# Optimization experiments

Hardware: AMD Instinct MI355X
Metric: run time of the kernel (lower is better)

Reference implementation:

```python
import jax, jax.numpy as jnp
import numpy as np

B, S, D, H = 2, 2048, 1024, 16
HD = D // H

def setup_inputs() -> dict:
    key = jax.random.key(0)
    ks = jax.random.split(key, 5)
    s = 1.0 / np.sqrt(D)
    return {
        "x": jax.random.normal(ks[0], (B, S, D), dtype=jnp.float32),
        "Wq": jax.random.normal(ks[1], (D, D), dtype=jnp.float32) * s,
        "Wk": jax.random.normal(ks[2], (D, D), dtype=jnp.float32) * s,
        "Wv": jax.random.normal(ks[3], (D, D), dtype=jnp.float32) * s,
        "Wo": jax.random.normal(ks[4], (D, D), dtype=jnp.float32) * s,
        "bo": jnp.zeros((D,), dtype=jnp.float32),
    }

def reference(x, Wq, Wk, Wv, Wo, bo):
    b, n, _ = x.shape
    # QKV projections (no bias), reshape to [B, H, S, HD]
    def proj(W):
        return (x @ W.T).reshape(b, n, H, HD).transpose(0, 2, 1, 3)
    q, k, v = proj(Wq), proj(Wk), proj(Wv)
    scores = jnp.einsum("bhqd,bhkd->bhqk", q, k)
    causal = jnp.triu(jnp.ones((n, n), dtype=bool), k=1)
    scores = jnp.where(causal, -jnp.inf, scores)
    attn = jax.nn.softmax(scores / np.sqrt(HD), axis=-1)  # dropout p=0.0 (eval)
    ctx = jnp.einsum("bhqk,bhkd->bhqd", attn, v)
    ctx = ctx.transpose(0, 2, 1, 3).reshape(b, n, D)
    return ctx @ Wo.T + bo
```

## Files before the change

kernel.cpp:

```cpp
#include <hip/hip_runtime.h>
#include <stdint.h>


typedef __bf16 bf16_t;
typedef __bf16 bf16x8 __attribute__((ext_vector_type(8)));
typedef float  f32x4  __attribute__((ext_vector_type(4)));
typedef uint32_t u32x4 __attribute__((ext_vector_type(4)));

#define MFMA16(A, B, C) __builtin_amdgcn_mfma_f32_16x16x32_bf16(A, B, C, 0, 0, 0)

__device__ __forceinline__ void async_ld16(const bf16_t* g, bf16_t* l) {
  __builtin_amdgcn_global_load_lds(
      (const __attribute__((address_space(1))) void*)g,
      (__attribute__((address_space(3))) void*)l, 16, 0, 0);
}

__global__ __launch_bounds__(256) void cvt_all(
    const float* __restrict__ sx, const float* __restrict__ s1,
    const float* __restrict__ s2, const float* __restrict__ s3,
    bf16_t* __restrict__ dx, bf16_t* __restrict__ d1,
    bf16_t* __restrict__ d2, bf16_t* __restrict__ d3) {
  const int y = blockIdx.y;
  if (y != 0 && blockIdx.x >= 1024) return;
  const int i4 = (blockIdx.x * 256 + threadIdx.x) * 4;
  const float* s = (y == 0) ? sx : (y == 1) ? s1 : (y == 2) ? s2 : s3;
  bf16_t*      d = (y == 0) ? dx : (y == 1) ? d1 : (y == 2) ? d2 : d3;
  const float4 v = *(const float4*)(s + i4);
  union { uint64_t u; bf16_t h[4]; } pk;
  pk.h[0] = (bf16_t)v.x; pk.h[1] = (bf16_t)v.y;
  pk.h[2] = (bf16_t)v.z; pk.h[3] = (bf16_t)v.w;
  *(uint64_t*)(d + i4) = pk.u;
}

__global__ __launch_bounds__(256) void cvt_wo(
    const float* __restrict__ s, bf16_t* __restrict__ d) {
  const int i4 = (blockIdx.x * 256 + threadIdx.x) * 4;
  const float4 v = *(const float4*)(s + i4);
  union { uint64_t u; bf16_t h[4]; } pk;
  pk.h[0] = (bf16_t)v.x; pk.h[1] = (bf16_t)v.y;
  pk.h[2] = (bf16_t)v.z; pk.h[3] = (bf16_t)v.w;
  *(uint64_t*)(d + i4) = pk.u;
}

__global__ __launch_bounds__(256, 3) void gemm_qkv_a(
    const bf16_t* __restrict__ X,  const bf16_t* __restrict__ Wq,
    const bf16_t* __restrict__ Wk, const bf16_t* __restrict__ Wv,
    bf16_t* __restrict__ Q, bf16_t* __restrict__ K, bf16_t* __restrict__ V) {
  const int z = blockIdx.z;
  const bf16_t* W = (z == 0) ? Wq : (z == 1) ? Wk : Wv;
  bf16_t*       D = (z == 0) ? Q  : (z == 1) ? K  : V;
  const int mode = (z == 2) ? 1 : 0;

  __shared__ __align__(16) bf16_t As[128 * 64];
  __shared__ __align__(16) bf16_t Bs[128 * 64];

  const int tid  = threadIdx.x;
  const int lane = tid & 63;
  const int w    = tid >> 6;
  const int quad = lane >> 4;
  const int l15  = lane & 15;
  const int bm   = blockIdx.y * 128;
  const int bn   = blockIdx.x * 128;
  const int wm   = (w >> 1) * 64;
  const int wn   = (w & 1) * 64;
  const int sr   = lane >> 3;
  const int sc   = lane & 7;

  f32x4 acc[4][4] = {};

  for (int k0 = 0; k0 < 1024; k0 += 64) {
#pragma unroll
    for (int j = 0; j < 4; ++j) {
      const int r0 = w * 32 + j * 8;
      const int r  = r0 + sr;
      const int c  = sc ^ (r & 7);
      async_ld16(X + (size_t)(bm + r) * 1024 + k0 + c * 8, &As[r0 * 64]);
      async_ld16(W + (size_t)(bn + r) * 1024 + k0 + c * 8, &Bs[r0 * 64]);
    }
    __syncthreads();
#pragma unroll
    for (int kk = 0; kk < 64; kk += 32) {
      const int ck = (kk >> 3) + quad;
      bf16x8 aF[4], bF[4];
#pragma unroll
      for (int mt = 0; mt < 4; ++mt) {
        const int r = wm + mt * 16 + l15;
        aF[mt] = *(const bf16x8*)&As[r * 64 + (ck ^ (r & 7)) * 8];
      }
#pragma unroll
      for (int nt = 0; nt < 4; ++nt) {
        const int r = wn + nt * 16 + l15;
        bF[nt] = *(const bf16x8*)&Bs[r * 64 + (ck ^ (r & 7)) * 8];
      }
#pragma unroll
      for (int mt = 0; mt < 4; ++mt)
#pragma unroll
        for (int nt = 0; nt < 4; ++nt)
          acc[mt][nt] = MFMA16(aF[mt], bF[nt], acc[mt][nt]);
    }
    __syncthreads();
  }

#pragma unroll
  for (int mt = 0; mt < 4; ++mt) {
#pragma unroll
    for (int nt = 0; nt < 4; ++nt) {
      const int n  = bn + wn + nt * 16 + l15;
      const int mb = bm + wm + mt * 16 + quad * 4;
      const int h = n >> 6, hd = n & 63;
      if (mode == 0) {
#pragma unroll
        for (int r = 0; r < 4; ++r) {
          const int m = mb + r;
          const int b = m >> 11, s = m & 2047;
          D[(size_t)b * 2097152 + (size_t)h * 131072 + (size_t)s * 64 + hd] =
              (bf16_t)acc[mt][nt][r];
        }
      } else {
        const int b = mb >> 11, s0 = mb & 2047;
        union { uint64_t u; bf16_t h4[4]; } pk;
#pragma unroll
        for (int r = 0; r < 4; ++r) pk.h4[r] = (bf16_t)acc[mt][nt][r];
        *(uint64_t*)(D + (size_t)b * 2097152 + (size_t)h * 131072 +
                     (size_t)hd * 2048 + s0) = pk.u;
      }
    }
  }
}

__global__ __launch_bounds__(256, 2) void gemm_out_a(
    const bf16_t* __restrict__ ctx, const bf16_t* __restrict__ Wob,
    float* __restrict__ out, const float* __restrict__ bo) {
  __shared__ __align__(16) bf16_t As[64 * 64];
  __shared__ __align__(16) bf16_t Bs[128 * 64];

  const int tid  = threadIdx.x;
  const int lane = tid & 63;
  const int w    = tid >> 6;
  const int quad = lane >> 4;
  const int l15  = lane & 15;
  const int bm   = blockIdx.y * 64;
  const int bn   = blockIdx.x * 128;
  const int wm   = (w >> 1) * 32;
  const int wn   = (w & 1) * 64;
  const int sr   = lane >> 3;
  const int sc   = lane & 7;

  f32x4 acc[2][4] = {};

  for (int k0 = 0; k0 < 1024; k0 += 64) {
#pragma unroll
    for (int j = 0; j < 2; ++j) {
      const int r0 = w * 16 + j * 8;
      const int r  = r0 + sr;
      const int c  = sc ^ (r & 7);
      async_ld16(ctx + (size_t)(bm + r) * 1024 + k0 + c * 8, &As[r0 * 64]);
    }
#pragma unroll
    for (int j = 0; j < 4; ++j) {
      const int r0 = w * 32 + j * 8;
      const int r  = r0 + sr;
      const int c  = sc ^ (r & 7);
      async_ld16(Wob + (size_t)(bn + r) * 1024 + k0 + c * 8, &Bs[r0 * 64]);
    }
    __syncthreads();
#pragma unroll
    for (int kk = 0; kk < 64; kk += 32) {
      const int ck = (kk >> 3) + quad;
      bf16x8 aF[2], bF[4];
#pragma unroll
      for (int mt = 0; mt < 2; ++mt) {
        const int r = wm + mt * 16 + l15;
        aF[mt] = *(const bf16x8*)&As[r * 64 + (ck ^ (r & 7)) * 8];
      }
#pragma unroll
      for (int nt = 0; nt < 4; ++nt) {
        const int r = wn + nt * 16 + l15;
        bF[nt] = *(const bf16x8*)&Bs[r * 64 + (ck ^ (r & 7)) * 8];
      }
#pragma unroll
      for (int mt = 0; mt < 2; ++mt)
#pragma unroll
        for (int nt = 0; nt < 4; ++nt)
          acc[mt][nt] = MFMA16(aF[mt], bF[nt], acc[mt][nt]);
    }
    __syncthreads();
  }

#pragma unroll
  for (int mt = 0; mt < 2; ++mt) {
#pragma unroll
    for (int nt = 0; nt < 4; ++nt) {
      const int n  = bn + wn + nt * 16 + l15;
      const int mb = bm + wm + mt * 16 + quad * 4;
      const float bv = bo[n];
#pragma unroll
      for (int r = 0; r < 4; ++r)
        out[(size_t)(mb + r) * 1024 + n] = acc[mt][nt][r] + bv;
    }
  }
}

__global__ __launch_bounds__(256, 4) void attn(
    const bf16_t* __restrict__ Qw, const bf16_t* __restrict__ Kw,
    const bf16_t* __restrict__ Vw, bf16_t* __restrict__ ctx) {
  constexpr int LDK = 72, LDV = 72, LDP = 72;
  __shared__ __align__(16) bf16_t Ks[64 * LDK];
  __shared__ __align__(16) bf16_t Vts[64 * LDV];
  __shared__ __align__(16) bf16_t Ps[64 * LDP];

  const int tid  = threadIdx.x;
  const int lane = tid & 63;
  const int w    = tid >> 6;
  const int quad = lane >> 4;
  const int l15  = lane & 15;
  const int h    = blockIdx.y;
  const int b    = blockIdx.z;
  const int x    = blockIdx.x;
  const int u    = (b << 1) | ((h >> 3) & 1);
  const int r64  = (u == 0) ? x
                 : (u == 1) ? (31 - x)
                 : (u == 2) ? ((x + 16) & 31)
                            : ((15 - x) & 31);
  const size_t bh = (size_t)(b * 16 + h) * (size_t)(2048 * 64);
  const bf16_t* Qh = Qw + bh;
  const bf16_t* Kh = Kw + bh;
  const bf16_t* Vh = Vw + bh;

  const int srl = lane >> 3, scl = lane & 7;

  {
    const int srow = tid >> 3, sch = tid & 7;
    u32x4 rq[2];
#pragma unroll
    for (int s2 = 0; s2 < 2; ++s2)
      rq[s2] = *(const u32x4*)(Qh + (size_t)(r64 * 64 + srow + s2 * 32) * 64 + sch * 8);
#pragma unroll
    for (int s2 = 0; s2 < 2; ++s2)
      *(u32x4*)&Ps[(srow + s2 * 32) * LDP + sch * 8] = rq[s2];
  }
  __syncthreads();
  bf16x8 qF[2];
#pragma unroll
  for (int k2 = 0; k2 < 2; ++k2)
    qF[k2] = *(const bf16x8*)&Ps[(w * 16 + l15) * LDP + k2 * 32 + quad * 8];

  f32x4 O[4] = {};
  float mrow = -1e30f, lrow = 0.f;
  const float sc_log2 = 0.125f * 1.44269504088896340736f;
  const float DTHR = 44.0f;

  u32x4 rk[2], rv[2];
#pragma unroll
  for (int j = 0; j < 2; ++j)
    rk[j] = *(const u32x4*)(Kh + (size_t)(w * 16 + j * 8 + srl) * 64 + scl * 8);
#pragma unroll
  for (int j = 0; j < 2; ++j)
    rv[j] = *(const u32x4*)(Vh + (size_t)(w * 16 + j * 8 + srl) * 2048 + scl * 8);

  for (int kt = 0; kt <= r64; ++kt) {
    __syncthreads();
#pragma unroll
    for (int j = 0; j < 2; ++j)
      *(u32x4*)&Ks[(w * 16 + j * 8 + srl) * LDK + scl * 8] = rk[j];
#pragma unroll
    for (int j = 0; j < 2; ++j)
      *(u32x4*)&Vts[(w * 16 + j * 8 + srl) * LDV + scl * 8] = rv[j];
    __syncthreads();

    if (kt < r64) {
      const int kn = kt + 1;
#pragma unroll
      for (int j = 0; j < 2; ++j)
        rk[j] = *(const u32x4*)(Kh + (size_t)(kn * 64 + w * 16 + j * 8 + srl) * 64 + scl * 8);
#pragma unroll
      for (int j = 0; j < 2; ++j)
        rv[j] = *(const u32x4*)(Vh + (size_t)(w * 16 + j * 8 + srl) * 2048 + kn * 64 + scl * 8);
    }

    f32x4 St[4] = {};
    __builtin_amdgcn_s_setprio(1);
#pragma unroll
    for (int ntk = 0; ntk < 4; ++ntk) {
      const int kr = ntk * 16 + l15;
#pragma unroll
      for (int k2 = 0; k2 < 2; ++k2) {
        const bf16x8 kF = *(const bf16x8*)&Ks[kr * LDK + k2 * 32 + quad * 8];
        St[ntk] = MFMA16(kF, qF[k2], St[ntk]);
      }
    }
    __builtin_amdgcn_s_setprio(0);

    if (kt == r64) {
      const int ql = w * 16 + l15;
#pragma unroll
      for (int ntk = 0; ntk < 4; ++ntk)
#pragma unroll
        for (int r = 0; r < 4; ++r)
          if (ntk * 16 + quad * 4 + r > ql) St[ntk][r] = -1e30f;
    }

    float mx = -1e30f;
#pragma unroll
    for (int ntk = 0; ntk < 4; ++ntk)
#pragma unroll
      for (int r = 0; r < 4; ++r) mx = fmaxf(mx, St[ntk][r]);
    mx = fmaxf(mx, __shfl_xor(mx, 16));
    mx = fmaxf(mx, __shfl_xor(mx, 32));

    float alpha = 1.f;
    if (!__all(mx - mrow <= DTHR)) {
      const float mnew = fmaxf(mrow, mx);
      alpha = exp2f((mrow - mnew) * sc_log2);
      mrow = mnew;
#pragma unroll
      for (int r = 0; r < 4; ++r) {
        const float a = __shfl(alpha, quad * 4 + r);
#pragma unroll
        for (int nt = 0; nt < 4; ++nt) O[nt][r] *= a;
      }
    }

    float rs = 0.f;
#pragma unroll
    for (int ntk = 0; ntk < 4; ++ntk) {
      union { uint64_t u64; bf16_t h4[4]; } pk;
#pragma unroll
      for (int r = 0; r < 4; ++r) {
        const float p = exp2f((St[ntk][r] - mrow) * sc_log2);
        rs += p;
        pk.h4[r] = (bf16_t)p;
      }
      *(uint64_t*)&Ps[(w * 16 + l15) * LDP + ntk * 16 + quad * 4] = pk.u64;
    }
    rs += __shfl_xor(rs, 16);
    rs += __shfl_xor(rs, 32);
    lrow = lrow * alpha + rs;

    __builtin_amdgcn_s_setprio(1);
#pragma unroll
    for (int kk = 0; kk < 64; kk += 32) {
      const int co = kk + quad * 8;
      const bf16x8 pF = *(const bf16x8*)&Ps[(w * 16 + l15) * LDP + co];
      bf16x8 vF[4];
#pragma unroll
      for (int nt = 0; nt < 4; ++nt)
        vF[nt] = *(const bf16x8*)&Vts[(nt * 16 + l15) * LDV + co];
#pragma unroll
      for (int nt = 0; nt < 4; ++nt)
        O[nt] = MFMA16(pF, vF[nt], O[nt]);
    }
    __builtin_amdgcn_s_setprio(0);
  }

#pragma unroll
  for (int r = 0; r < 4; ++r) {
    const float lr = __shfl(lrow, quad * 4 + r);
    const float iv = 1.f / lr;
    const int s = r64 * 64 + w * 16 + quad * 4 + r;
#pragma unroll
    for (int nt = 0; nt < 4; ++nt) {
      const int hd = nt * 16 + l15;
      ctx[(size_t)(b * 2048 + s) * 1024 + h * 64 + hd] =
          (bf16_t)(O[nt][r] * iv);
    }
  }
}

extern "C" void kernel_launch(void* const* d_in, const int* in_sizes, int n_in,
                              void* d_out, int out_size, void* d_ws, size_t ws_size,
                              hipStream_t stream) {
  const float* x  = (const float*)d_in[0];
  const float* Wq = (const float*)d_in[1];
  const float* Wk = (const float*)d_in[2];
  const float* Wv = (const float*)d_in[3];
  const float* Wo = (const float*)d_in[4];
  const float* bo = (const float*)d_in[5];

  bf16_t* ws   = (bf16_t*)d_ws;
  bf16_t* Qw   = ws;
  bf16_t* Kw   = ws + 4194304;
  bf16_t* Vw   = ws + 8388608;
  bf16_t* ctxw = ws + 12582912;
  bf16_t* Wob  = Qw;

  bf16_t* dscr = (bf16_t*)d_out;
  bf16_t* xb   = dscr;
  bf16_t* Wqb  = dscr + 4194304;
  bf16_t* Wkb  = dscr + 5242880;
  bf16_t* Wvb  = dscr + 6291456;
  float*  out  = (float*)d_out;

  dim3 blk(256);
  cvt_all<<<dim3(4096, 4), blk, 0, stream>>>(x, Wq, Wk, Wv, xb, Wqb, Wkb, Wvb);
  gemm_qkv_a<<<dim3(8, 32, 3), blk, 0, stream>>>(xb, Wqb, Wkb, Wvb, Qw, Kw, Vw);
  attn<<<dim3(32, 16, 2), blk, 0, stream>>>(Qw, Kw, Vw, ctxw);
  cvt_wo<<<dim3(1024), blk, 0, stream>>>(Wo, Wob);
  gemm_out_a<<<dim3(8, 64), blk, 0, stream>>>(ctxw, Wob, out, bo);
}
```

Measured before the change: 181.4 us.

## Double-buffer attention K/V tiles with async global-to-LDS loads and XOR swizzle

Replaces the register-staged K/V prefetch in the attention kernel with direct global_load_lds async copies into double-buffered LDS tiles, waiting with explicit vmcnt counts. The padded LDS layout is replaced by an XOR-swizzled 64-wide layout for K, V and P to avoid bank conflicts without padding. Q fragments are now loaded straight from global memory instead of through LDS. This removes register pressure and the per-iteration LDS store pass, at the cost of doubling K/V LDS usage and relying on hand-written waitcnt/barrier ordering.

```diff
diff --git a/kernel.cpp b/kernel.cpp
--- a/kernel.cpp
+++ b/kernel.cpp
@@ -204,10 +204,9 @@
 __global__ __launch_bounds__(256, 4) void attn(
     const bf16_t* __restrict__ Qw, const bf16_t* __restrict__ Kw,
     const bf16_t* __restrict__ Vw, bf16_t* __restrict__ ctx) {
-  constexpr int LDK = 72, LDV = 72, LDP = 72;
-  __shared__ __align__(16) bf16_t Ks[64 * LDK];
-  __shared__ __align__(16) bf16_t Vts[64 * LDV];
-  __shared__ __align__(16) bf16_t Ps[64 * LDP];
+  __shared__ __align__(16) bf16_t Kb[2][64 * 64];
+  __shared__ __align__(16) bf16_t Vb[2][64 * 64];
+  __shared__ __align__(16) bf16_t Ps[64 * 64];
 
   const int tid  = threadIdx.x;
   const int lane = tid & 63;
@@ -228,64 +227,67 @@
   const bf16_t* Vh = Vw + bh;
 
   const int srl = lane >> 3, scl = lane & 7;
-
+  const int swl = scl ^ srl;
+
+  bf16x8 qF[2];
   {
-    const int srow = tid >> 3, sch = tid & 7;
-    u32x4 rq[2];
-#pragma unroll
-    for (int s2 = 0; s2 < 2; ++s2)
-      rq[s2] = *(const u32x4*)(Qh + (size_t)(r64 * 64 + srow + s2 * 32) * 64 + sch * 8);
-#pragma unroll
-    for (int s2 = 0; s2 < 2; ++s2)
-      *(u32x4*)&Ps[(srow + s2 * 32) * LDP + sch * 8] = rq[s2];
-  }
-  __syncthreads();
-  bf16x8 qF[2];
-#pragma unroll
-  for (int k2 = 0; k2 < 2; ++k2)
-    qF[k2] = *(const bf16x8*)&Ps[(w * 16 + l15) * LDP + k2 * 32 + quad * 8];
+    const bf16_t* qrow = Qh + (size_t)(r64 * 64 + w * 16 + l15) * 64 + quad * 8;
+#pragma unroll
+    for (int k2 = 0; k2 < 2; ++k2) qF[k2] = *(const bf16x8*)(qrow + k2 * 32);
+  }
+
+#pragma unroll
+  for (int j = 0; j < 2; ++j) {
+    const int r0 = w * 16 + j * 8;
+    async_ld16(Kh + (size_t)(r0 + srl) * 64 + swl * 8, &Kb[0][r0 * 64]);
+  }
+#pragma unroll
+  for (int j = 0; j < 2; ++j) {
+    const int r0 = w * 16 + j * 8;
+    async_ld16(Vh + (size_t)(r0 + srl) * 2048 + swl * 8, &Vb[0][r0 * 64]);
+  }
 
   f32x4 O[4] = {};
   float mrow = -1e30f, lrow = 0.f;
   const float sc_log2 = 0.125f * 1.44269504088896340736f;
   const float DTHR = 44.0f;
 
-  u32x4 rk[2], rv[2];
-#pragma unroll
-  for (int j = 0; j < 2; ++j)
-    rk[j] = *(const u32x4*)(Kh + (size_t)(w * 16 + j * 8 + srl) * 64 + scl * 8);
-#pragma unroll
-  for (int j = 0; j < 2; ++j)
-    rv[j] = *(const u32x4*)(Vh + (size_t)(w * 16 + j * 8 + srl) * 2048 + scl * 8);
-
   for (int kt = 0; kt <= r64; ++kt) {
-    __syncthreads();
-#pragma unroll
-    for (int j = 0; j < 2; ++j)
-      *(u32x4*)&Ks[(w * 16 + j * 8 + srl) * LDK + scl * 8] = rk[j];
-#pragma unroll
-    for (int j = 0; j < 2; ++j)
-      *(u32x4*)&Vts[(w * 16 + j * 8 + srl) * LDV + scl * 8] = rv[j];
-    __syncthreads();
-
+    const int cur = kt & 1;
+    asm volatile("" ::: "memory");
+    __builtin_amdgcn_s_barrier();
+    asm volatile("" ::: "memory");
     if (kt < r64) {
       const int kn = kt + 1;
 #pragma unroll
-      for (int j = 0; j < 2; ++j)
-        rk[j] = *(const u32x4*)(Kh + (size_t)(kn * 64 + w * 16 + j * 8 + srl) * 64 + scl * 8);
-#pragma unroll
-      for (int j = 0; j < 2; ++j)
-        rv[j] = *(const u32x4*)(Vh + (size_t)(w * 16 + j * 8 + srl) * 2048 + kn * 64 + scl * 8);
-    }
+      for (int j = 0; j < 2; ++j) {
+        const int r0 = w * 16 + j * 8;
+        async_ld16(Kh + (size_t)(kn * 64 + r0 + srl) * 64 + swl * 8,
+                   &Kb[cur ^ 1][r0 * 64]);
+      }
+#pragma unroll
+      for (int j = 0; j < 2; ++j) {
+        const int r0 = w * 16 + j * 8;
+        async_ld16(Vh + (size_t)(r0 + srl) * 2048 + kn * 64 + swl * 8,
+                   &Vb[cur ^ 1][r0 * 64]);
+      }
+      asm volatile("s_waitcnt vmcnt(4)" ::: "memory");
+    } else {
+      asm volatile("s_waitcnt vmcnt(0)" ::: "memory");
+    }
+    __builtin_amdgcn_s_barrier();
+    asm volatile("" ::: "memory");
 
     f32x4 St[4] = {};
     __builtin_amdgcn_s_setprio(1);
 #pragma unroll
     for (int ntk = 0; ntk < 4; ++ntk) {
       const int kr = ntk * 16 + l15;
+      const int sw = l15 & 7;
 #pragma unroll
       for (int k2 = 0; k2 < 2; ++k2) {
-        const bf16x8 kF = *(const bf16x8*)&Ks[kr * LDK + k2 * 32 + quad * 8];
+        const bf16x8 kF = *(const bf16x8*)
+            &Kb[cur][kr * 64 + (((k2 << 2) | quad) ^ sw) * 8];
         St[ntk] = MFMA16(kF, qF[k2], St[ntk]);
       }
     }
@@ -322,6 +324,8 @@
     }
 
     float rs = 0.f;
+    const int prow = w * 16 + l15;
+    const int psw  = l15 & 7;
 #pragma unroll
     for (int ntk = 0; ntk < 4; ++ntk) {
       union { uint64_t u64; bf16_t h4[4]; } pk;
@@ -331,7 +335,8 @@
         rs += p;
         pk.h4[r] = (bf16_t)p;
       }
-      *(uint64_t*)&Ps[(w * 16 + l15) * LDP + ntk * 16 + quad * 4] = pk.u64;
+      *(uint64_t*)&Ps[prow * 64 + (((2 * ntk + (quad >> 1)) ^ psw) * 8) +
+                      (quad & 1) * 4] = pk.u64;
     }
     rs += __shfl_xor(rs, 16);
     rs += __shfl_xor(rs, 32);
@@ -340,12 +345,14 @@
     __builtin_amdgcn_s_setprio(1);
 #pragma unroll
     for (int kk = 0; kk < 64; kk += 32) {
-      const int co = kk + quad * 8;
-      const bf16x8 pF = *(const bf16x8*)&Ps[(w * 16 + l15) * LDP + co];
+      const int ck = ((kk >> 3) + quad);
+      const bf16x8 pF = *(const bf16x8*)&Ps[prow * 64 + ((ck ^ psw) * 8)];
       bf16x8 vF[4];
 #pragma unroll
-      for (int nt = 0; nt < 4; ++nt)
-        vF[nt] = *(const bf16x8*)&Vts[(nt * 16 + l15) * LDV + co];
+      for (int nt = 0; nt < 4; ++nt) {
+        const int vr = nt * 16 + l15;
+        vF[nt] = *(const bf16x8*)&Vb[cur][vr * 64 + ((ck ^ (l15 & 7)) * 8)];
+      }
 #pragma unroll
       for (int nt = 0; nt < 4; ++nt)
         O[nt] = MFMA16(pF, vF[nt], O[nt]);
```

New measurement: 192.0 us. 1.06x slower.
